# Kernel optimization log

Measured on AMD Instinct MI355X. Metric: run time of the kernel, lower is better.

## Reference

```python
import jax, jax.numpy as jnp
import numpy as np
from jax import lax

# Rotation permutations for a flattened 3x3 kernel (row-major, new_flat[t] = orig_flat[perm[t]]),
# transcribed literally from _rotate_kernel for n = angle//45 in {0,1,2,3}.
PERMS = np.array([
    [0, 1, 2, 3, 4, 5, 6, 7, 8],  # 0 deg (identity)
    [3, 0, 1, 6, 4, 2, 7, 8, 5],  # 45 deg: outer ring shifted one step
    [6, 3, 0, 7, 4, 1, 8, 5, 2],  # 90 deg clockwise
    [7, 6, 3, 8, 4, 0, 5, 2, 1],  # 135 deg
], dtype=np.int32)


def setup_inputs() -> dict:
    key = jax.random.key(0)
    k1, k2, k3 = jax.random.split(key, 3)
    B, Cin, Cout, H, W = 16, 64, 64, 128, 128
    x = jax.random.normal(k1, (B, Cin, H, W), dtype=jnp.float32)
    weight = jax.random.normal(k2, (Cout, Cin, 3, 3), dtype=jnp.float32)
    bias = jax.random.normal(k3, (Cout, 1, 1), dtype=jnp.float32)
    return {"x": x, "weight": weight, "bias": bias}


def reference(x, weight, bias):
    # x: [B, Cin, H, W]; weight: [Cout, Cin, 3, 3]; bias: [Cout, 1, 1]
    B, Cin, H, W = x.shape
    Cout = weight.shape[0]
    n_ang = PERMS.shape[0]

    # Build the 4 rotated kernel variants in one gather.
    wflat = weight.reshape(Cout, Cin, 9)
    # [Cout, Cin, n_ang, 9] -> [n_ang, Cout, Cin, 3, 3] -> merge angle into output channels
    wrot = wflat[:, :, jnp.asarray(PERMS)].transpose(2, 0, 1, 3).reshape(n_ang * Cout, Cin, 3, 3)

    # ZeroPad2d(stride=1) then valid 3x3 conv -> same spatial size.
    xp = jnp.pad(x, ((0, 0), (0, 0), (1, 1), (1, 1)))
    y = lax.conv_general_dilated(
        xp, wrot, window_strides=(1, 1), padding="VALID",
        dimension_numbers=("NCHW", "OIHW", "NCHW"))  # [B, n_ang*Cout, H, W]

    y = y.reshape(B, n_ang, Cout, H, W).transpose(1, 0, 2, 3, 4)  # [n_ang, B, Cout, H, W]
    return y + bias  # bias (Cout,1,1) broadcasts over trailing dims
```

## Files before the change

### kernel.cpp

```cpp
#include <hip/hip_runtime.h>


#define CIN 64
#define COUT 64
#define HH 128
#define WW 128
#define NB 16
#define HW (HH*WW)

typedef short bf16x8 __attribute__((ext_vector_type(8)));
typedef float f32x16 __attribute__((ext_vector_type(16)));
#define AS1 __attribute__((address_space(1)))
#define AS3 __attribute__((address_space(3)))

__device__ __constant__ unsigned APERM_d[4][9] = {
  {0,8192,16384,24576,32768,40960,49152,57344,65536},
  {24576,0,8192,49152,32768,16384,57344,65536,40960},
  {49152,24576,0,57344,32768,8192,65536,40960,16384},
  {57344,49152,24576,65536,32768,0,40960,16384,8192},
};

static __device__ __forceinline__ unsigned short f2bf(float f) {
  unsigned u = __builtin_bit_cast(unsigned, f);
  return (unsigned short)((u + 0x7FFFu + ((u >> 16) & 1u)) >> 16);
}
static __device__ __forceinline__ unsigned pk2(float lo, float hi) {
  return (unsigned)f2bf(lo) | ((unsigned)f2bf(hi) << 16);
}

__global__ void build_A_kernel(const float* __restrict__ wgt,
                               const float* __restrict__ bias,
                               unsigned short* __restrict__ A) {
  const int e = blockIdx.x * 256 + threadIdx.x;
  const int j = e & 7;
  const int cm = (e >> 3) & 63;
  const int half = (e >> 9) & 1;
  const int kc = e >> 10;
  if (kc < 36) {
    const int s = kc >> 2, q = kc & 3;
    const int ci = q * 16 + half * 8 + j;
    A[e] = f2bf(wgt[(cm * CIN + ci) * 9 + s]);
  } else if (kc == 36) {
    A[e] = (half == 0 && j == 0) ? f2bf(bias[cm]) : (unsigned short)0;
  }
}

#define XS_SLOT 2080
#define XS_ROW  16640
#define XS_OFF  75776
#define LDS_BYTES (XS_OFF + 4 * XS_ROW)

__global__ __launch_bounds__(1024, 4) void aconv_v13_kernel(
    const float* __restrict__ x,
    const unsigned short* __restrict__ Ag,
    float* __restrict__ out)
{
  __shared__ __align__(16) unsigned char lds[LDS_BYTES];

  const int tid = threadIdx.x;
  const int lane = tid & 63;
  const int wid = tid >> 6;
  const int a   = __builtin_amdgcn_readfirstlane(wid >> 2);
  const int row = __builtin_amdgcn_readfirstlane((wid >> 1) & 1);
  const int wh  = __builtin_amdgcn_readfirstlane(wid & 1);
  const int half = lane >> 5;
  const int ln = lane & 31;

  const int b   = blockIdx.x >> 4;
  const int rem = blockIdx.x & 15;
  const int hbase = rem * 8;

  const unsigned char* Agb = (const unsigned char*)Ag;
  AS3 unsigned char* ldsa = (AS3 unsigned char*)lds;
  const uint4 z4 = {0u, 0u, 0u, 0u};

  #pragma unroll
  for (int j = 0; j < 5; ++j) {
    const int i = wid + j * 16;
    if (i < 74)
      __builtin_amdgcn_global_load_lds(
          (const AS1 unsigned*)(Agb + i * 1024 + lane * 16),
          (AS3 unsigned*)(ldsa + i * 1024), 16, 0, 0);
  }
  if (tid < 64) {
    const int rs = tid >> 4, cs = (tid >> 1) & 7, side = tid & 1;
    *(uint4*)(lds + XS_OFF + rs * XS_ROW + cs * XS_SLOT + side * 129 * 16) = z4;
  }

  const int sslot = (tid >> 7) & 7;
  const int swc   = tid & 127;
  const float* sxb = x + (size_t)(b * CIN + sslot * 8) * HW + swc;
  const unsigned sdstb = (unsigned)(XS_OFF + sslot * XS_SLOT + (1 + swc) * 16);

  #pragma unroll
  for (int i = 0; i < 4; ++i) {
    const int gh = hbase - 1 + i;
    const bool inb = (unsigned)gh < HH;
    const float* xp = sxb + (size_t)gh * WW;
    float v[8];
    #pragma unroll
    for (int q = 0; q < 8; ++q) v[q] = inb ? xp[(size_t)q * HW] : 0.f;
    uint4 u;
    u.x = pk2(v[0], v[1]); u.y = pk2(v[2], v[3]);
    u.z = pk2(v[4], v[5]); u.w = pk2(v[6], v[7]);
    *(uint4*)(lds + sdstb + i * XS_ROW) = u;
  }
  __syncthreads();

  float gv[2][8];
  #pragma unroll
  for (int i = 0; i < 2; ++i) {
    const int gh = hbase + 3 + i;
    const bool inb = (unsigned)gh < HH;
    const float* xp = sxb + (size_t)gh * WW;
    #pragma unroll
    for (int q = 0; q < 8; ++q) gv[i][q] = inb ? xp[(size_t)q * HW] : 0.f;
  }

  const unsigned char* Asb = lds + (unsigned)(half * 1024 + ln * 16);
  const unsigned char* Bsb = lds + XS_OFF + (unsigned)(half * XS_SLOT + (wh * 64 + ln) * 16);

  bf16x8 ob = (bf16x8)(short)0;
  if (half == 0) ob[0] = (short)0x3F80;

  #pragma unroll 1
  for (int it = 0; it < 4; ++it) {
    const int rowbase = it * 2 + row;
    unsigned ro[3];
    #pragma unroll
    for (int dh = 0; dh < 3; ++dh)
      ro[dh] = (unsigned)(((rowbase + dh) & 3) * XS_ROW);

    f32x16 acc[2][2];
    #pragma unroll
    for (int mf = 0; mf < 2; ++mf)
      #pragma unroll
      for (int nf = 0; nf < 2; ++nf) acc[mf][nf] = (f32x16)(0.f);

    #pragma unroll
    for (int t = 0; t < 9; ++t) {
      if (t == 6) {
        asm volatile("s_waitcnt lgkmcnt(0)" ::: "memory");
        __builtin_amdgcn_s_barrier();
        if (it < 3) {
          #pragma unroll
          for (int i = 0; i < 2; ++i) {
            const int gh = hbase + it * 2 + 3 + i;
            uint4 u = z4;
            if (gh < HH) {
              u.x = pk2(gv[i][0], gv[i][1]); u.y = pk2(gv[i][2], gv[i][3]);
              u.z = pk2(gv[i][4], gv[i][5]); u.w = pk2(gv[i][6], gv[i][7]);
            }
            *(uint4*)(lds + sdstb + (unsigned)(((it * 2 + i) & 3) * XS_ROW)) = u;
          }
        }
      }
      const unsigned aoff = APERM_d[a][t];
      const unsigned bbt = ro[t / 3] + (unsigned)((t % 3) * 16);
      #pragma unroll
      for (int q = 0; q < 4; ++q) {
        const bf16x8 af0 = *(const bf16x8*)(Asb + aoff + q * 2048);
        const bf16x8 af1 = *(const bf16x8*)(Asb + aoff + q * 2048 + 512);
        const unsigned bb = bbt + (unsigned)(q * 2 * XS_SLOT);
        const bf16x8 bf0 = *(const bf16x8*)(Bsb + bb);
        const bf16x8 bf1 = *(const bf16x8*)(Bsb + bb + 512);
        acc[0][0] = __builtin_amdgcn_mfma_f32_32x32x16_bf16(af0, bf0, acc[0][0], 0, 0, 0);
        acc[0][1] = __builtin_amdgcn_mfma_f32_32x32x16_bf16(af0, bf1, acc[0][1], 0, 0, 0);
        acc[1][0] = __builtin_amdgcn_mfma_f32_32x32x16_bf16(af1, bf0, acc[1][0], 0, 0, 0);
        acc[1][1] = __builtin_amdgcn_mfma_f32_32x32x16_bf16(af1, bf1, acc[1][1], 0, 0, 0);
      }
    }
    {
      const bf16x8 af0 = *(const bf16x8*)(Asb + 36 * 2048);
      const bf16x8 af1 = *(const bf16x8*)(Asb + 36 * 2048 + 512);
      acc[0][0] = __builtin_amdgcn_mfma_f32_32x32x16_bf16(af0, ob, acc[0][0], 0, 0, 0);
      acc[0][1] = __builtin_amdgcn_mfma_f32_32x32x16_bf16(af0, ob, acc[0][1], 0, 0, 0);
      acc[1][0] = __builtin_amdgcn_mfma_f32_32x32x16_bf16(af1, ob, acc[1][0], 0, 0, 0);
      acc[1][1] = __builtin_amdgcn_mfma_f32_32x32x16_bf16(af1, ob, acc[1][1], 0, 0, 0);
    }

    if (it < 2) {
      #pragma unroll
      for (int i = 0; i < 2; ++i) {
        const int gh = hbase + it * 2 + 5 + i;
        const bool inb = (unsigned)gh < HH;
        const float* xp = sxb + (size_t)gh * WW;
        #pragma unroll
        for (int q = 0; q < 8; ++q) gv[i][q] = inb ? xp[(size_t)q * HW] : 0.f;
      }
    }

    const int hout = hbase + it * 2 + row;
    #pragma unroll
    for (int mf = 0; mf < 2; ++mf)
      #pragma unroll
      for (int nf = 0; nf < 2; ++nf) {
        const f32x16 v = acc[mf][nf];
        float* op = out + (((size_t)(a * NB + b) * COUT + mf * 32 + 4 * half) * HH
                           + hout) * WW + wh * 64 + nf * 32 + ln;
        #pragma unroll
        for (int g = 0; g < 16; ++g)
          __builtin_nontemporal_store(v[g], op + (size_t)((g & 3) + 8 * (g >> 2)) * HW);
      }

    asm volatile("s_waitcnt lgkmcnt(0)" ::: "memory");
    __builtin_amdgcn_s_barrier();
  }
}

extern "C" void kernel_launch(void* const* d_in, const int* in_sizes, int n_in,
                              void* d_out, int out_size, void* d_ws, size_t ws_size,
                              hipStream_t stream) {
  const float* x    = (const float*)d_in[0];
  const float* wgt  = (const float*)d_in[1];
  const float* bias = (const float*)d_in[2];
  float* out = (float*)d_out;
  unsigned short* A = (unsigned short*)d_ws;

  build_A_kernel<<<148, 256, 0, stream>>>(wgt, bias, A);
  aconv_v13_kernel<<<256, 1024, 0, stream>>>(x, A, out);
}
```

Baseline: 107.7 us.

## Halve block to 512 threads, loop over width halves, fold bias into accumulator init

Each block now runs 8 waves instead of 16, and every wave loops over both width halves. This doubles the MFMA work per wave and cuts the waves per block. Bias is no longer applied by an extra MFMA against a ones-vector; it is loaded into registers and used to initialise the accumulators. The padded-input staging is restructured so all threads fill the halo columns and rows, and the next-row prefetch and LDS refill happen every other iteration behind two barriers. The trade is less parallelism per block and more registers per wave (bias and prefetch buffers), with less sync and no bias MFMA.

```diff
diff --git a/kernel.cpp b/kernel.cpp
--- a/kernel.cpp
+++ b/kernel.cpp
@@ -29,30 +29,31 @@
 }
 
 __global__ void build_A_kernel(const float* __restrict__ wgt,
-                               const float* __restrict__ bias,
                                unsigned short* __restrict__ A) {
   const int e = blockIdx.x * 256 + threadIdx.x;
   const int j = e & 7;
   const int cm = (e >> 3) & 63;
   const int half = (e >> 9) & 1;
   const int kc = e >> 10;
-  if (kc < 36) {
-    const int s = kc >> 2, q = kc & 3;
-    const int ci = q * 16 + half * 8 + j;
-    A[e] = f2bf(wgt[(cm * CIN + ci) * 9 + s]);
-  } else if (kc == 36) {
-    A[e] = (half == 0 && j == 0) ? f2bf(bias[cm]) : (unsigned short)0;
-  }
+  const int s = kc >> 2, q = kc & 3;
+  const int ci = q * 16 + half * 8 + j;
+  A[e] = f2bf(wgt[(cm * CIN + ci) * 9 + s]);
+}
+
+static __device__ __forceinline__ void lgkm_barrier() {
+  asm volatile("s_waitcnt lgkmcnt(0)" ::: "memory");
+  __builtin_amdgcn_s_barrier();
 }
 
 #define XS_SLOT 2080
 #define XS_ROW  16640
-#define XS_OFF  75776
+#define XS_OFF  73728
 #define LDS_BYTES (XS_OFF + 4 * XS_ROW)
 
-__global__ __launch_bounds__(1024, 4) void aconv_v13_kernel(
+__global__ __launch_bounds__(512) void aconv_v14_kernel(
     const float* __restrict__ x,
     const unsigned short* __restrict__ Ag,
+    const float* __restrict__ bias,
     float* __restrict__ out)
 {
   __shared__ __align__(16) unsigned char lds[LDS_BYTES];
@@ -60,9 +61,8 @@
   const int tid = threadIdx.x;
   const int lane = tid & 63;
   const int wid = tid >> 6;
-  const int a   = __builtin_amdgcn_readfirstlane(wid >> 2);
-  const int row = __builtin_amdgcn_readfirstlane((wid >> 1) & 1);
-  const int wh  = __builtin_amdgcn_readfirstlane(wid & 1);
+  const int a   = wid >> 1;
+  const int row = wid & 1;
   const int half = lane >> 5;
   const int ln = lane & 31;
 
@@ -75,88 +75,93 @@
   const uint4 z4 = {0u, 0u, 0u, 0u};
 
   #pragma unroll
-  for (int j = 0; j < 5; ++j) {
-    const int i = wid + j * 16;
-    if (i < 74)
-      __builtin_amdgcn_global_load_lds(
-          (const AS1 unsigned*)(Agb + i * 1024 + lane * 16),
-          (AS3 unsigned*)(ldsa + i * 1024), 16, 0, 0);
+  for (int j = 0; j < 9; ++j) {
+    const int i = wid + j * 8;
+    __builtin_amdgcn_global_load_lds(
+        (const AS1 unsigned*)(Agb + i * 1024 + lane * 16),
+        (AS3 unsigned*)(ldsa + i * 1024), 16, 0, 0);
   }
-  if (tid < 64) {
-    const int rs = tid >> 4, cs = (tid >> 1) & 7, side = tid & 1;
-    *(uint4*)(lds + XS_OFF + rs * XS_ROW + cs * XS_SLOT + side * 129 * 16) = z4;
-  }
-
-  const int sslot = (tid >> 7) & 7;
-  const int swc   = tid & 127;
-  const float* sxb = x + (size_t)(b * CIN + sslot * 8) * HW + swc;
-  const unsigned sdstb = (unsigned)(XS_OFF + sslot * XS_SLOT + (1 + swc) * 16);
-
+
+  float bv[2][16];
   #pragma unroll
-  for (int i = 0; i < 4; ++i) {
-    const int gh = hbase - 1 + i;
-    const bool inb = (unsigned)gh < HH;
-    const float* xp = sxb + (size_t)gh * WW;
-    float v[8];
-    #pragma unroll
-    for (int q = 0; q < 8; ++q) v[q] = inb ? xp[(size_t)q * HW] : 0.f;
-    uint4 u;
-    u.x = pk2(v[0], v[1]); u.y = pk2(v[2], v[3]);
-    u.z = pk2(v[4], v[5]); u.w = pk2(v[6], v[7]);
-    *(uint4*)(lds + sdstb + i * XS_ROW) = u;
+  for (int mf = 0; mf < 2; ++mf)
+    #pragma unroll
+    for (int g = 0; g < 16; ++g)
+      bv[mf][g] = bias[mf * 32 + (g & 3) + 8 * (g >> 2) + 4 * half];
+
+  #pragma unroll
+  for (int i = 0; i < 9; ++i) {
+    const int g = tid + i * 512;
+    if (g < 4160) {
+      const int r    = g / 1040;
+      const int rest = g - r * 1040;
+      const int slot = rest / 130;
+      const int wI   = rest - slot * 130;
+      const int gh = hbase - 1 + r;
+      const int gw = wI - 1;
+      const bool inb = ((unsigned)gh < HH) && ((unsigned)gw < WW);
+      const float* xp = x + (size_t)(b * CIN + slot * 8) * HW + (size_t)gh * WW + gw;
+      float v[8];
+      #pragma unroll
+      for (int q = 0; q < 8; ++q) v[q] = inb ? xp[(size_t)q * HW] : 0.f;
+      uint4 u;
+      u.x = pk2(v[0], v[1]); u.y = pk2(v[2], v[3]);
+      u.z = pk2(v[4], v[5]); u.w = pk2(v[6], v[7]);
+      *(uint4*)(lds + XS_OFF + r * XS_ROW + slot * XS_SLOT + wI * 16) = u;
+    }
   }
   __syncthreads();
 
-  float gv[2][8];
-  #pragma unroll
-  for (int i = 0; i < 2; ++i) {
-    const int gh = hbase + 3 + i;
-    const bool inb = (unsigned)gh < HH;
-    const float* xp = sxb + (size_t)gh * WW;
-    #pragma unroll
-    for (int q = 0; q < 8; ++q) gv[i][q] = inb ? xp[(size_t)q * HW] : 0.f;
-  }
-
   const unsigned char* Asb = lds + (unsigned)(half * 1024 + ln * 16);
-  const unsigned char* Bsb = lds + XS_OFF + (unsigned)(half * XS_SLOT + (wh * 64 + ln) * 16);
-
-  bf16x8 ob = (bf16x8)(short)0;
-  if (half == 0) ob[0] = (short)0x3F80;
+  const unsigned char* Bsb = lds + XS_OFF + (unsigned)(half * XS_SLOT + ln * 16);
+
+  float gv[5][8];
 
   #pragma unroll 1
-  for (int it = 0; it < 4; ++it) {
-    const int rowbase = it * 2 + row;
+  for (int ti = 0; ti < 8; ++ti) {
+    const int it = ti >> 1;
+    const int wh = ti & 1;
+    const bool odd = (wh == 1);
+    const bool rst = odd && (it < 3);
+
     unsigned ro[3];
     #pragma unroll
     for (int dh = 0; dh < 3; ++dh)
-      ro[dh] = (unsigned)(((rowbase + dh) & 3) * XS_ROW);
+      ro[dh] = (unsigned)(((it * 2 + row + dh) & 3) * XS_ROW);
+
+    if (rst) {
+      #pragma unroll
+      for (int i = 0; i < 5; ++i) {
+        const int g = tid + i * 512;
+        if (g < 2080) {
+          const int rr   = g / 1040;
+          const int rest = g - rr * 1040;
+          const int slot = rest / 130;
+          const int wI   = rest - slot * 130;
+          const int gh = hbase + it * 2 + 3 + rr;
+          const int gw = wI - 1;
+          const bool inb = ((unsigned)gh < HH) && ((unsigned)gw < WW);
+          const float* xp = x + (size_t)(b * CIN + slot * 8) * HW + (size_t)gh * WW + gw;
+          #pragma unroll
+          for (int q = 0; q < 8; ++q) gv[i][q] = inb ? xp[(size_t)q * HW] : 0.f;
+        }
+      }
+    }
 
     f32x16 acc[2][2];
     #pragma unroll
     for (int mf = 0; mf < 2; ++mf)
       #pragma unroll
-      for (int nf = 0; nf < 2; ++nf) acc[mf][nf] = (f32x16)(0.f);
-
+      for (int nf = 0; nf < 2; ++nf)
+        #pragma unroll
+        for (int g = 0; g < 16; ++g)
+          acc[mf][nf][g] = bv[mf][g];
+
+    const unsigned whb = (unsigned)(wh * 64 * 16);
     #pragma unroll
     for (int t = 0; t < 9; ++t) {
-      if (t == 6) {
-        asm volatile("s_waitcnt lgkmcnt(0)" ::: "memory");
-        __builtin_amdgcn_s_barrier();
-        if (it < 3) {
-          #pragma unroll
-          for (int i = 0; i < 2; ++i) {
-            const int gh = hbase + it * 2 + 3 + i;
-            uint4 u = z4;
-            if (gh < HH) {
-              u.x = pk2(gv[i][0], gv[i][1]); u.y = pk2(gv[i][2], gv[i][3]);
-              u.z = pk2(gv[i][4], gv[i][5]); u.w = pk2(gv[i][6], gv[i][7]);
-            }
-            *(uint4*)(lds + sdstb + (unsigned)(((it * 2 + i) & 3) * XS_ROW)) = u;
-          }
-        }
-      }
       const unsigned aoff = APERM_d[a][t];
-      const unsigned bbt = ro[t / 3] + (unsigned)((t % 3) * 16);
+      const unsigned bbt = ro[t / 3] + (unsigned)((t % 3) * 16) + whb;
       #pragma unroll
       for (int q = 0; q < 4; ++q) {
         const bf16x8 af0 = *(const bf16x8*)(Asb + aoff + q * 2048);
@@ -170,25 +175,6 @@
         acc[1][1] = __builtin_amdgcn_mfma_f32_32x32x16_bf16(af1, bf1, acc[1][1], 0, 0, 0);
       }
     }
-    {
-      const bf16x8 af0 = *(const bf16x8*)(Asb + 36 * 2048);
-      const bf16x8 af1 = *(const bf16x8*)(Asb + 36 * 2048 + 512);
-      acc[0][0] = __builtin_amdgcn_mfma_f32_32x32x16_bf16(af0, ob, acc[0][0], 0, 0, 0);
-      acc[0][1] = __builtin_amdgcn_mfma_f32_32x32x16_bf16(af0, ob, acc[0][1], 0, 0, 0);
-      acc[1][0] = __builtin_amdgcn_mfma_f32_32x32x16_bf16(af1, ob, acc[1][0], 0, 0, 0);
-      acc[1][1] = __builtin_amdgcn_mfma_f32_32x32x16_bf16(af1, ob, acc[1][1], 0, 0, 0);
-    }
-
-    if (it < 2) {
-      #pragma unroll
-      for (int i = 0; i < 2; ++i) {
-        const int gh = hbase + it * 2 + 5 + i;
-        const bool inb = (unsigned)gh < HH;
-        const float* xp = sxb + (size_t)gh * WW;
-        #pragma unroll
-        for (int q = 0; q < 8; ++q) gv[i][q] = inb ? xp[(size_t)q * HW] : 0.f;
-      }
-    }
 
     const int hout = hbase + it * 2 + row;
     #pragma unroll
@@ -203,8 +189,25 @@
           __builtin_nontemporal_store(v[g], op + (size_t)((g & 3) + 8 * (g >> 2)) * HW);
       }
 
-    asm volatile("s_waitcnt lgkmcnt(0)" ::: "memory");
-    __builtin_amdgcn_s_barrier();
+    if (rst) {
+      lgkm_barrier();
+      #pragma unroll
+      for (int i = 0; i < 5; ++i) {
+        const int g = tid + i * 512;
+        if (g < 2080) {
+          const int rr   = g / 1040;
+          const int rest = g - rr * 1040;
+          const int slot = rest / 130;
+          const int wI   = rest - slot * 130;
+          uint4 u;
+          u.x = pk2(gv[i][0], gv[i][1]); u.y = pk2(gv[i][2], gv[i][3]);
+          u.z = pk2(gv[i][4], gv[i][5]); u.w = pk2(gv[i][6], gv[i][7]);
+          *(uint4*)(lds + XS_OFF + (unsigned)(((it * 2 + 4 + rr) & 3) * XS_ROW)
+                    + slot * XS_SLOT + wI * 16) = u;
+        }
+      }
+      lgkm_barrier();
+    }
   }
 }
 
@@ -217,6 +220,6 @@
   float* out = (float*)d_out;
   unsigned short* A = (unsigned short*)d_ws;
 
-  build_A_kernel<<<148, 256, 0, stream>>>(wgt, bias, A);
-  aconv_v13_kernel<<<256, 1024, 0, stream>>>(x, A, out);
-}
+  build_A_kernel<<<144, 256, 0, stream>>>(wgt, A);
+  aconv_v14_kernel<<<256, 512, 0, stream>>>(x, A, bias, out);
+}
```

New measurement: 98.40 us. 1.09x faster.
